# Optimization experiments

Measured on AMD Instinct MI355X. Metric: run time of the kernel, lower is better.

The kernel has to match this reference:

```python
import jax, jax.numpy as jnp
import numpy as np

N_NODES = 100000
N_EDGES = 1600000
F_IN = 256
HEADS1, DIM1 = 8, 8
N_CLASSES = 16
NEG_SLOPE = 0.2  # LeakyReLU slope used by GAT attention


def _gat_layer(x, src, dst, W, a_src, a_dst, n_nodes):
    """Graph attention layer (Velickovic et al.).
    x: [N, Fin], W: [Fin, H*D], a_src/a_dst: [H, D]. Returns [N, H, D].
    """
    H, D = a_src.shape
    h = (x @ W).reshape(-1, H, D)                      # [N, H, D]
    s = jnp.einsum('nhd,hd->nh', h, a_src)             # [N, H]
    t = jnp.einsum('nhd,hd->nh', h, a_dst)             # [N, H]
    e = jax.nn.leaky_relu(s[src] + t[dst], NEG_SLOPE)  # [E, H] per-edge logits
    # numerically stable segment softmax over incoming edges of each dst node
    m = jax.ops.segment_max(e, dst, num_segments=n_nodes)
    m = jnp.where(jnp.isfinite(m), m, 0.0)
    ex = jnp.exp(e - m[dst])                           # [E, H]
    denom = jax.ops.segment_sum(ex, dst, num_segments=n_nodes)
    alpha = ex / (denom[dst] + 1e-16)                  # [E, H]
    # gather source features, weight by attention, scatter-add to dst
    out = jax.ops.segment_sum(alpha[:, :, None] * h[src], dst,
                              num_segments=n_nodes)    # [N, H, D]
    return out


def setup_inputs() -> dict:
    key = jax.random.key(0)
    ks = jax.random.split(key, 8)
    x = jax.random.normal(ks[0], (N_NODES, F_IN), dtype=jnp.float32)
    edge_index = jax.random.randint(ks[1], (2, N_EDGES), 0, N_NODES, dtype=jnp.int64)
    W1 = jax.random.normal(ks[2], (F_IN, HEADS1 * DIM1), dtype=jnp.float32) * 0.1
    a1_src = jax.random.normal(ks[3], (HEADS1, DIM1), dtype=jnp.float32) * 0.1
    a1_dst = jax.random.normal(ks[4], (HEADS1, DIM1), dtype=jnp.float32) * 0.1
    W2 = jax.random.normal(ks[5], (HEADS1 * DIM1, N_CLASSES), dtype=jnp.float32) * 0.1
    a2_src = jax.random.normal(ks[6], (1, N_CLASSES), dtype=jnp.float32) * 0.1
    a2_dst = jax.random.normal(ks[7], (1, N_CLASSES), dtype=jnp.float32) * 0.1
    return {"x": x, "edge_index": edge_index, "W1": W1, "a1_src": a1_src,
            "a1_dst": a1_dst, "W2": W2, "a2_src": a2_src, "a2_dst": a2_dst}


def reference(x, edge_index, W1, a1_src, a1_dst, W2, a2_src, a2_dst):
    # eval mode: dropout(p=0.6) layers are identity
    src, dst = edge_index[0], edge_index[1]
    h1 = _gat_layer(x, src, dst, W1, a1_src, a1_dst, N_NODES)   # [N, 8, 8]
    h1 = jax.nn.elu(h1.reshape(N_NODES, HEADS1 * DIM1))         # concat heads
    h2 = _gat_layer(h1, src, dst, W2, a2_src, a2_dst, N_NODES)  # [N, 1, C]
    logits = h2.reshape(N_NODES, N_CLASSES)
    return jax.nn.log_softmax(logits, axis=1)
```

## Files before the change

kernel.cpp:

```cpp
#include <hip/hip_runtime.h>
#include <math.h>

#define N_NODES 100000
#define N_EDGES 1600000
#define NHEAD   8
#define NC      16
#define NEG     0.2f
#define BSH     8
#define NBUCK   391
#define CAP     5120
#define TILE2   4096
#define NBLK2   391

typedef __attribute__((ext_vector_type(4))) float f32x4;
typedef __attribute__((ext_vector_type(8))) short s16x8;

__device__ __forceinline__ float lrelu(float x) { return x > 0.f ? x : NEG * x; }
__device__ __forceinline__ short bf16rne(float f) {
    unsigned u = __float_as_uint(f);
    return (short)((u + 0x7FFFu + ((u >> 16) & 1u)) >> 16);
}
__device__ __forceinline__ float bf2f(unsigned short u) {
    return __uint_as_float(((unsigned)u) << 16);
}

__global__ __launch_bounds__(256) void wtrans_kernel(const float* __restrict__ W1,
                                                     float4* __restrict__ Wt) {
    int u = blockIdx.x * 256 + threadIdx.x;
    int j = u >> 9, ks = (u >> 6) & 7, l = u & 63;
    int colc = j * 16 + (l & 15);
    int k0 = ks * 32 + (l >> 4) * 8;
    union { s16x8 s; float4 f; } pk;
#pragma unroll
    for (int i = 0; i < 8; ++i) pk.s[i] = bf16rne(W1[(size_t)(k0 + i) * 64 + colc]);
    Wt[u] = pk.f;
}

__global__ __launch_bounds__(256) void gemm1_kernel(
    const float* __restrict__ x, const float4* __restrict__ Wt,
    const float* __restrict__ a1s, const float* __restrict__ a1d,
    unsigned short* __restrict__ hb, float* __restrict__ s, float* __restrict__ t) {
    __shared__ float4 WtL[2048];
    int tid = threadIdx.x;
#pragma unroll
    for (int i = 0; i < 8; ++i) WtL[tid + i * 256] = Wt[tid + i * 256];
    int w = tid >> 6, lane = tid & 63;
    int n0 = blockIdx.x * 128;
    int r0 = n0 + w * 32 + (lane & 15);
    int r1 = r0 + 16;
    int cr0 = r0 < N_NODES ? r0 : 0;
    int cr1 = r1 < N_NODES ? r1 : 0;
    int koff = (lane >> 4) * 8;
    f32x4 acc[2][4];
#pragma unroll
    for (int r = 0; r < 2; ++r)
#pragma unroll
        for (int j = 0; j < 4; ++j) acc[r][j] = (f32x4)0.f;
    __syncthreads();
#pragma unroll
    for (int ks = 0; ks < 8; ++ks) {
        const float* p0 = x + (size_t)cr0 * 256 + ks * 32 + koff;
        const float* p1 = x + (size_t)cr1 * 256 + ks * 32 + koff;
        float4 a0l = *(const float4*)p0, a0h = *(const float4*)(p0 + 4);
        float4 a1l = *(const float4*)p1, a1h = *(const float4*)(p1 + 4);
        s16x8 A0, A1;
        A0[0] = bf16rne(a0l.x); A0[1] = bf16rne(a0l.y); A0[2] = bf16rne(a0l.z); A0[3] = bf16rne(a0l.w);
        A0[4] = bf16rne(a0h.x); A0[5] = bf16rne(a0h.y); A0[6] = bf16rne(a0h.z); A0[7] = bf16rne(a0h.w);
        A1[0] = bf16rne(a1l.x); A1[1] = bf16rne(a1l.y); A1[2] = bf16rne(a1l.z); A1[3] = bf16rne(a1l.w);
        A1[4] = bf16rne(a1h.x); A1[5] = bf16rne(a1h.y); A1[6] = bf16rne(a1h.z); A1[7] = bf16rne(a1h.w);
#pragma unroll
        for (int j = 0; j < 4; ++j) {
            s16x8 B = *(s16x8*)&WtL[(j * 8 + ks) * 64 + lane];
            acc[0][j] = __builtin_amdgcn_mfma_f32_16x16x32_bf16(A0, B, acc[0][j], 0, 0, 0);
            acc[1][j] = __builtin_amdgcn_mfma_f32_16x16x32_bf16(A1, B, acc[1][j], 0, 0, 0);
        }
    }
    float asv[4], adv[4];
#pragma unroll
    for (int j = 0; j < 4; ++j) {
        int c = j * 16 + (lane & 15);
        asv[j] = a1s[c]; adv[j] = a1d[c];
    }
    int rbase = (lane >> 4) * 4;
#pragma unroll
    for (int r = 0; r < 2; ++r) {
#pragma unroll
        for (int reg = 0; reg < 4; ++reg) {
            int grow = n0 + w * 32 + r * 16 + rbase + reg;
            bool live = grow < N_NODES;
            unsigned short* hp = hb + (size_t)grow * 64 + (lane & 15);
#pragma unroll
            for (int j = 0; j < 4; ++j) {
                float hv = acc[r][j][reg];
                if (live) hp[j * 16] = (unsigned short)bf16rne(hv);
                float ps = hv * asv[j];
                float pt = hv * adv[j];
                ps += __shfl_xor(ps, 1, 64); ps += __shfl_xor(ps, 2, 64); ps += __shfl_xor(ps, 4, 64);
                pt += __shfl_xor(pt, 1, 64); pt += __shfl_xor(pt, 2, 64); pt += __shfl_xor(pt, 4, 64);
                if ((lane & 7) == 0 && live) {
                    int head = 2 * j + ((lane >> 3) & 1);
                    s[grow * 8 + head] = ps;
                    t[grow * 8 + head] = pt;
                }
            }
        }
    }
}

__global__ __launch_bounds__(512) void binscatter_kernel(
    const int* __restrict__ esrc, const int* __restrict__ edst,
    int* __restrict__ bcur, unsigned* __restrict__ tmp) {
    __shared__ unsigned buf[TILE2];
    __shared__ int hist[512], lbase[512], cur[512], gbase[512];
    int tid = threadIdx.x;
    hist[tid] = 0; cur[tid] = 0;
    __syncthreads();
    int e0 = blockIdx.x * TILE2;
#pragma unroll
    for (int k = 0; k < TILE2 / 512; ++k) {
        int e = e0 + k * 512 + tid;
        if (e < N_EDGES) atomicAdd(&hist[edst[e] >> BSH], 1);
    }
    __syncthreads();
    int v = hist[tid];
    lbase[tid] = v;
    __syncthreads();
    for (int off = 1; off < 512; off <<= 1) {
        int a = (tid >= off) ? lbase[tid - off] : 0;
        __syncthreads();
        lbase[tid] += a;
        __syncthreads();
    }
    lbase[tid] -= v;
    gbase[tid] = v ? atomicAdd(&bcur[tid], v) : 0;
    __syncthreads();
#pragma unroll
    for (int k = 0; k < TILE2 / 512; ++k) {
        int e = e0 + k * 512 + tid;
        if (e < N_EDGES) {
            int d = edst[e];
            int b = d >> BSH;
            int p = lbase[b] + atomicAdd(&cur[b], 1);
            buf[p] = (unsigned)esrc[e] | ((unsigned)(d & ((1 << BSH) - 1)) << 17);
        }
    }
    __syncthreads();
    int w = tid >> 6, lane = tid & 63;
    for (int b = w; b < 512; b += 8) {
        int L = hist[b];
        if (!L) continue;
        int lb = lbase[b];
        size_t base = (size_t)b * CAP + gbase[b];
        for (int i = lane; i < L; i += 64) tmp[base + i] = buf[lb + i];
    }
}

__global__ __launch_bounds__(256) void bsort_kernel(
    const int* __restrict__ bcur, const unsigned* __restrict__ tmp,
    int* __restrict__ rowbeg, int* __restrict__ rowend, int* __restrict__ colslab) {
    __shared__ unsigned sorted[CAP];
    __shared__ int cnt[256], scn[256];
    int tid = threadIdx.x, b = blockIdx.x;
    int L = bcur[b];
    const unsigned* tb = tmp + (size_t)b * CAP;
    cnt[tid] = 0;
    __syncthreads();
    for (int i = tid; i < L; i += 256) atomicAdd(&cnt[tb[i] >> 17], 1);
    __syncthreads();
    int v = cnt[tid];
    scn[tid] = v;
    __syncthreads();
    for (int off = 1; off < 256; off <<= 1) {
        int a = (tid >= off) ? scn[tid - off] : 0;
        __syncthreads();
        scn[tid] += a;
        __syncthreads();
    }
    int ex = scn[tid] - v;
    int node = (b << BSH) + tid;
    if (node < N_NODES) {
        rowbeg[node] = b * CAP + ex;
        rowend[node] = b * CAP + ex + v;
    }
    cnt[tid] = ex;
    __syncthreads();
    for (int i = tid; i < L; i += 256) {
        unsigned u = tb[i];
        int p = atomicAdd(&cnt[u >> 17], 1);
        sorted[p] = u & 0x1FFFFu;
    }
    __syncthreads();
    for (int i = tid; i < L; i += 256) colslab[(size_t)b * CAP + i] = (int)sorted[i];
}

__global__ __launch_bounds__(256) void agg1_kernel(
    const int* __restrict__ rowbeg, const int* __restrict__ rowend,
    const int* __restrict__ colslab,
    const float* __restrict__ s, const float* __restrict__ t,
    const unsigned short* __restrict__ hb, unsigned short* __restrict__ h1b) {
    int tid = threadIdx.x;
    int d = __builtin_amdgcn_readfirstlane(blockIdx.x * 4 + (tid >> 6));
    int lane = tid & 63, hh = lane >> 3;
    int beg = rowbeg[d], end = rowend[d];
    unsigned len = (unsigned)(end - beg);
    float tv = t[d * 8 + hh];
    float acc0 = 0.f, acc1 = 0.f, acc2 = 0.f, acc3 = 0.f;
    float den0 = 0.f, den1 = 0.f, den2 = 0.f, den3 = 0.f;
    for (int p = beg & ~3; p < end; p += 4) {
        int4 c4 = *(const int4*)(colslab + p);
        {
            bool ok = (unsigned)(p - beg) < len;
            int s0 = c4.x & 0x1FFFF; if (s0 >= N_NODES) s0 = 0;
            float e = __expf(lrelu(s[s0 * 8 + hh] + tv));
            e = ok ? e : 0.f;
            acc0 += e * bf2f(hb[(size_t)s0 * 64 + lane]); den0 += e;
        }
        {
            bool ok = (unsigned)(p + 1 - beg) < len;
            int s0 = c4.y & 0x1FFFF; if (s0 >= N_NODES) s0 = 0;
            float e = __expf(lrelu(s[s0 * 8 + hh] + tv));
            e = ok ? e : 0.f;
            acc1 += e * bf2f(hb[(size_t)s0 * 64 + lane]); den1 += e;
        }
        {
            bool ok = (unsigned)(p + 2 - beg) < len;
            int s0 = c4.z & 0x1FFFF; if (s0 >= N_NODES) s0 = 0;
            float e = __expf(lrelu(s[s0 * 8 + hh] + tv));
            e = ok ? e : 0.f;
            acc2 += e * bf2f(hb[(size_t)s0 * 64 + lane]); den2 += e;
        }
        {
            bool ok = (unsigned)(p + 3 - beg) < len;
            int s0 = c4.w & 0x1FFFF; if (s0 >= N_NODES) s0 = 0;
            float e = __expf(lrelu(s[s0 * 8 + hh] + tv));
            e = ok ? e : 0.f;
            acc3 += e * bf2f(hb[(size_t)s0 * 64 + lane]); den3 += e;
        }
    }
    float v = (acc0 + acc1 + acc2 + acc3) / (den0 + den1 + den2 + den3 + 1e-16f);
    float r = v > 0.f ? v : __expf(v) - 1.f;
    h1b[(size_t)d * 64 + lane] = (unsigned short)bf16rne(r);
}

__global__ __launch_bounds__(256) void gemm2_kernel(
    const unsigned short* __restrict__ h1b, const float* __restrict__ W2,
    const float* __restrict__ a2s, const float* __restrict__ a2d,
    unsigned short* __restrict__ h2b, float* __restrict__ s2, float* __restrict__ t2) {
    __shared__ float Wl[64 * NC];
    __shared__ float h1l[16 * 65];
    int tid = threadIdx.x;
    ((float4*)Wl)[tid] = ((const float4*)W2)[tid];
    {
        uint2 raw = ((const uint2*)h1b)[(size_t)blockIdx.x * 256 + tid];
        int f = tid * 4, rr = f >> 6, kk = f & 63;
        float* dp = &h1l[rr * 65 + kk];
        dp[0] = __uint_as_float(raw.x << 16);
        dp[1] = __uint_as_float(raw.x & 0xFFFF0000u);
        dp[2] = __uint_as_float(raw.y << 16);
        dp[3] = __uint_as_float(raw.y & 0xFFFF0000u);
    }
    __syncthreads();
    int c = tid & 15, r = tid >> 4;
    int n = blockIdx.x * 16 + r;
    float a = 0.f;
#pragma unroll 16
    for (int k = 0; k < 64; ++k) a += h1l[r * 65 + k] * Wl[k * NC + c];
    h2b[(size_t)n * NC + c] = (unsigned short)bf16rne(a);
    float vs = a * a2s[c];
    float vt = a * a2d[c];
#pragma unroll
    for (int o = 1; o < 16; o <<= 1) {
        vs += __shfl_xor(vs, o, 64);
        vt += __shfl_xor(vt, o, 64);
    }
    if (c == 0) { s2[n] = vs; t2[n] = vt; }
}

__global__ __launch_bounds__(256) void agg2_kernel(
    const int* __restrict__ rowbeg, const int* __restrict__ rowend,
    const int* __restrict__ colslab,
    const float* __restrict__ s2, const float* __restrict__ t2,
    const unsigned short* __restrict__ h2b, float* __restrict__ out) {
    int tid = threadIdx.x;
    int d = blockIdx.x * 16 + (tid >> 4);
    int c = tid & 15;
    int beg = rowbeg[d], end = rowend[d];
    unsigned len = (unsigned)(end - beg);
    float tv = t2[d];
    float acc0 = 0.f, acc1 = 0.f, acc2 = 0.f, acc3 = 0.f;
    float den0 = 0.f, den1 = 0.f, den2 = 0.f, den3 = 0.f;
    for (int p = beg & ~3; p < end; p += 4) {
        int4 c4 = *(const int4*)(colslab + p);
        {
            bool ok = (unsigned)(p - beg) < len;
            int s0 = c4.x & 0x1FFFF; if (s0 >= N_NODES) s0 = 0;
            float e = __expf(lrelu(s2[s0] + tv));
            e = ok ? e : 0.f;
            acc0 += e * bf2f(h2b[(size_t)s0 * 16 + c]); den0 += e;
        }
        {
            bool ok = (unsigned)(p + 1 - beg) < len;
            int s0 = c4.y & 0x1FFFF; if (s0 >= N_NODES) s0 = 0;
            float e = __expf(lrelu(s2[s0] + tv));
            e = ok ? e : 0.f;
            acc1 += e * bf2f(h2b[(size_t)s0 * 16 + c]); den1 += e;
        }
        {
            bool ok = (unsigned)(p + 2 - beg) < len;
            int s0 = c4.z & 0x1FFFF; if (s0 >= N_NODES) s0 = 0;
            float e = __expf(lrelu(s2[s0] + tv));
            e = ok ? e : 0.f;
            acc2 += e * bf2f(h2b[(size_t)s0 * 16 + c]); den2 += e;
        }
        {
            bool ok = (unsigned)(p + 3 - beg) < len;
            int s0 = c4.w & 0x1FFFF; if (s0 >= N_NODES) s0 = 0;
            float e = __expf(lrelu(s2[s0] + tv));
            e = ok ? e : 0.f;
            acc3 += e * bf2f(h2b[(size_t)s0 * 16 + c]); den3 += e;
        }
    }
    float v = (acc0 + acc1 + acc2 + acc3) / (den0 + den1 + den2 + den3 + 1e-16f);
    float mx = v;
#pragma unroll
    for (int o = 1; o < 16; o <<= 1) mx = fmaxf(mx, __shfl_xor(mx, o, 64));
    float e = __expf(v - mx), sum = e;
#pragma unroll
    for (int o = 1; o < 16; o <<= 1) sum += __shfl_xor(sum, o, 64);
    out[(size_t)d * NC + c] = v - mx - __logf(sum);
}

extern "C" void kernel_launch(void* const* d_in, const int* in_sizes, int n_in,
                              void* d_out, int out_size, void* d_ws, size_t ws_size,
                              hipStream_t stream) {
    const float* x   = (const float*)d_in[0];
    const int*  eidx = (const int*)d_in[1];
    const float* W1  = (const float*)d_in[2];
    const float* a1s = (const float*)d_in[3];
    const float* a1d = (const float*)d_in[4];
    const float* W2  = (const float*)d_in[5];
    const float* a2s = (const float*)d_in[6];
    const float* a2d = (const float*)d_in[7];
    float* out = (float*)d_out;
    const int* esrc = eidx;
    const int* edst = eidx + N_EDGES;

    char* p = (char*)d_ws;
    int*      bcur    = (int*)p;      p += 512 * 4;
    unsigned* tmp     = (unsigned*)p; p += (size_t)NBUCK * CAP * 4;
    int*      colslab = (int*)p;      p += (size_t)NBUCK * CAP * 4 + 64;
    int*      rowbeg  = (int*)p;      p += (size_t)N_NODES * 4;
    int*      rowend  = (int*)p;      p += (size_t)N_NODES * 4;
    float4*   Wt      = (float4*)p;   p += (size_t)2048 * 16;
    unsigned short* hb  = (unsigned short*)p; p += (size_t)N_NODES * 64 * 2;
    float*    s       = (float*)p;    p += (size_t)N_NODES * 8 * 4;
    float*    t       = (float*)p;    p += (size_t)N_NODES * 8 * 4;
    unsigned short* h1b = (unsigned short*)p; p += (size_t)N_NODES * 64 * 2;
    unsigned short* h2b = (unsigned short*)p; p += (size_t)N_NODES * NC * 2;
    float*    s2      = (float*)p;    p += (size_t)N_NODES * 4;
    float*    t2      = (float*)p;    p += (size_t)N_NODES * 4;

    hipMemsetAsync(bcur, 0, 512 * 4, stream);

    wtrans_kernel<<<8, 256, 0, stream>>>(W1, Wt);
    gemm1_kernel<<<(N_NODES + 127) / 128, 256, 0, stream>>>(x, Wt, a1s, a1d, hb, s, t);
    binscatter_kernel<<<NBLK2, 512, 0, stream>>>(esrc, edst, bcur, tmp);
    bsort_kernel<<<NBUCK, 256, 0, stream>>>(bcur, tmp, rowbeg, rowend, colslab);
    agg1_kernel<<<N_NODES / 4, 256, 0, stream>>>(rowbeg, rowend, colslab, s, t, hb, h1b);
    gemm2_kernel<<<N_NODES / 16, 256, 0, stream>>>(h1b, W2, a2s, a2d, h2b, s2, t2);
    agg2_kernel<<<N_NODES / 16, 256, 0, stream>>>(rowbeg, rowend, colslab, s2, t2, h2b, out);
}
```

Measured before the change: 347.3 us.

## Compute edge softmax weights once per lane and broadcast via shuffles; use wave-shuffle scans

In both aggregation kernels, each lane now loads one edge's source index and computes that edge's attention exponent once. The values are then broadcast across the group with shuffles, where before every feature lane recomputed the exp and reloaded the score for every edge. This removes roughly 8x (layer 1) and 16x (layer 2) redundant exp and score gathers, at the cost of extra shuffle instructions and possible reads of colslab past the row end. Separately, the LDS Hillis-Steele prefix scans in the binning and bucket-sort kernels are replaced by in-wave shuffle scans plus a small per-wave sum, which cuts many block barriers.

After: 342.9 us. About the same (-1.3%).

```diff
diff --git a/kernel.cpp b/kernel.cpp
--- a/kernel.cpp
+++ b/kernel.cpp
@@ -111,7 +111,7 @@
     const int* __restrict__ esrc, const int* __restrict__ edst,
     int* __restrict__ bcur, unsigned* __restrict__ tmp) {
     __shared__ unsigned buf[TILE2];
-    __shared__ int hist[512], lbase[512], cur[512], gbase[512];
+    __shared__ int hist[512], lbase[512], cur[512], gbase[512], wsum[8];
     int tid = threadIdx.x;
     hist[tid] = 0; cur[tid] = 0;
     __syncthreads();
@@ -123,15 +123,18 @@
     }
     __syncthreads();
     int v = hist[tid];
-    lbase[tid] = v;
-    __syncthreads();
-    for (int off = 1; off < 512; off <<= 1) {
-        int a = (tid >= off) ? lbase[tid - off] : 0;
-        __syncthreads();
-        lbase[tid] += a;
-        __syncthreads();
-    }
-    lbase[tid] -= v;
+    int w = tid >> 6, lane = tid & 63;
+    int inc = v;
+#pragma unroll
+    for (int off = 1; off < 64; off <<= 1) {
+        int nb = __shfl_up(inc, off, 64);
+        if (lane >= off) inc += nb;
+    }
+    if (lane == 63) wsum[w] = inc;
+    __syncthreads();
+    int woff = 0;
+    for (int k = 0; k < w; ++k) woff += wsum[k];
+    lbase[tid] = inc - v + woff;
     gbase[tid] = v ? atomicAdd(&bcur[tid], v) : 0;
     __syncthreads();
 #pragma unroll
@@ -145,7 +148,6 @@
         }
     }
     __syncthreads();
-    int w = tid >> 6, lane = tid & 63;
     for (int b = w; b < 512; b += 8) {
         int L = hist[b];
         if (!L) continue;
@@ -159,7 +161,8 @@
     const int* __restrict__ bcur, const unsigned* __restrict__ tmp,
     int* __restrict__ rowbeg, int* __restrict__ rowend, int* __restrict__ colslab) {
     __shared__ unsigned sorted[CAP];
-    __shared__ int cnt[256], scn[256];
+    __shared__ int cnt[256];
+    __shared__ int wsum[4];
     int tid = threadIdx.x, b = blockIdx.x;
     int L = bcur[b];
     const unsigned* tb = tmp + (size_t)b * CAP;
@@ -168,15 +171,18 @@
     for (int i = tid; i < L; i += 256) atomicAdd(&cnt[tb[i] >> 17], 1);
     __syncthreads();
     int v = cnt[tid];
-    scn[tid] = v;
-    __syncthreads();
-    for (int off = 1; off < 256; off <<= 1) {
-        int a = (tid >= off) ? scn[tid - off] : 0;
-        __syncthreads();
-        scn[tid] += a;
-        __syncthreads();
-    }
-    int ex = scn[tid] - v;
+    int w = tid >> 6, lane = tid & 63;
+    int inc = v;
+#pragma unroll
+    for (int off = 1; off < 64; off <<= 1) {
+        int nb = __shfl_up(inc, off, 64);
+        if (lane >= off) inc += nb;
+    }
+    if (lane == 63) wsum[w] = inc;
+    __syncthreads();
+    int woff = 0;
+    for (int k = 0; k < w; ++k) woff += wsum[k];
+    int ex = inc - v + woff;
     int node = (b << BSH) + tid;
     if (node < N_NODES) {
         rowbeg[node] = b * CAP + ex;
@@ -200,44 +206,30 @@
     const unsigned short* __restrict__ hb, unsigned short* __restrict__ h1b) {
     int tid = threadIdx.x;
     int d = __builtin_amdgcn_readfirstlane(blockIdx.x * 4 + (tid >> 6));
-    int lane = tid & 63, hh = lane >> 3;
+    int lane = tid & 63;
+    int hh = lane >> 3;
+    int hA = lane & 7;
+    int sub = lane >> 3;
     int beg = rowbeg[d], end = rowend[d];
-    unsigned len = (unsigned)(end - beg);
-    float tv = t[d * 8 + hh];
-    float acc0 = 0.f, acc1 = 0.f, acc2 = 0.f, acc3 = 0.f;
-    float den0 = 0.f, den1 = 0.f, den2 = 0.f, den3 = 0.f;
-    for (int p = beg & ~3; p < end; p += 4) {
-        int4 c4 = *(const int4*)(colslab + p);
-        {
-            bool ok = (unsigned)(p - beg) < len;
-            int s0 = c4.x & 0x1FFFF; if (s0 >= N_NODES) s0 = 0;
-            float e = __expf(lrelu(s[s0 * 8 + hh] + tv));
-            e = ok ? e : 0.f;
-            acc0 += e * bf2f(hb[(size_t)s0 * 64 + lane]); den0 += e;
-        }
-        {
-            bool ok = (unsigned)(p + 1 - beg) < len;
-            int s0 = c4.y & 0x1FFFF; if (s0 >= N_NODES) s0 = 0;
-            float e = __expf(lrelu(s[s0 * 8 + hh] + tv));
-            e = ok ? e : 0.f;
-            acc1 += e * bf2f(hb[(size_t)s0 * 64 + lane]); den1 += e;
-        }
-        {
-            bool ok = (unsigned)(p + 2 - beg) < len;
-            int s0 = c4.z & 0x1FFFF; if (s0 >= N_NODES) s0 = 0;
-            float e = __expf(lrelu(s[s0 * 8 + hh] + tv));
-            e = ok ? e : 0.f;
-            acc2 += e * bf2f(hb[(size_t)s0 * 64 + lane]); den2 += e;
-        }
-        {
-            bool ok = (unsigned)(p + 3 - beg) < len;
-            int s0 = c4.w & 0x1FFFF; if (s0 >= N_NODES) s0 = 0;
-            float e = __expf(lrelu(s[s0 * 8 + hh] + tv));
-            e = ok ? e : 0.f;
-            acc3 += e * bf2f(hb[(size_t)s0 * 64 + lane]); den3 += e;
-        }
-    }
-    float v = (acc0 + acc1 + acc2 + acc3) / (den0 + den1 + den2 + den3 + 1e-16f);
+    float tvA = t[d * 8 + hA];
+    float acc[4] = {0.f, 0.f, 0.f, 0.f};
+    float den[4] = {0.f, 0.f, 0.f, 0.f};
+    for (int p = beg; p < end; p += 8) {
+        int pe = p + sub;
+        int s0 = colslab[pe];
+        if ((unsigned)s0 >= N_NODES) s0 = 0;
+        float ev = __expf(lrelu(s[s0 * 8 + hA] + tvA));
+        ev = (pe < end) ? ev : 0.f;
+#pragma unroll
+        for (int j = 0; j < 8; ++j) {
+            float e = __shfl(ev, j * 8 + hh, 64);
+            int sj  = __shfl(s0, j * 8, 64);
+            acc[j & 3] += e * bf2f(hb[(size_t)sj * 64 + lane]);
+            den[j & 3] += e;
+        }
+    }
+    float v = (acc[0] + acc[1] + acc[2] + acc[3])
+            / (den[0] + den[1] + den[2] + den[3] + 1e-16f);
     float r = v > 0.f ? v : __expf(v) - 1.f;
     h1b[(size_t)d * 64 + lane] = (unsigned short)bf16rne(r);
 }
@@ -283,44 +275,29 @@
     const unsigned short* __restrict__ h2b, float* __restrict__ out) {
     int tid = threadIdx.x;
     int d = blockIdx.x * 16 + (tid >> 4);
-    int c = tid & 15;
+    int lane = tid & 63;
+    int c = lane & 15;
+    int gb = lane & 48;
     int beg = rowbeg[d], end = rowend[d];
-    unsigned len = (unsigned)(end - beg);
     float tv = t2[d];
-    float acc0 = 0.f, acc1 = 0.f, acc2 = 0.f, acc3 = 0.f;
-    float den0 = 0.f, den1 = 0.f, den2 = 0.f, den3 = 0.f;
-    for (int p = beg & ~3; p < end; p += 4) {
-        int4 c4 = *(const int4*)(colslab + p);
-        {
-            bool ok = (unsigned)(p - beg) < len;
-            int s0 = c4.x & 0x1FFFF; if (s0 >= N_NODES) s0 = 0;
-            float e = __expf(lrelu(s2[s0] + tv));
-            e = ok ? e : 0.f;
-            acc0 += e * bf2f(h2b[(size_t)s0 * 16 + c]); den0 += e;
-        }
-        {
-            bool ok = (unsigned)(p + 1 - beg) < len;
-            int s0 = c4.y & 0x1FFFF; if (s0 >= N_NODES) s0 = 0;
-            float e = __expf(lrelu(s2[s0] + tv));
-            e = ok ? e : 0.f;
-            acc1 += e * bf2f(h2b[(size_t)s0 * 16 + c]); den1 += e;
-        }
-        {
-            bool ok = (unsigned)(p + 2 - beg) < len;
-            int s0 = c4.z & 0x1FFFF; if (s0 >= N_NODES) s0 = 0;
-            float e = __expf(lrelu(s2[s0] + tv));
-            e = ok ? e : 0.f;
-            acc2 += e * bf2f(h2b[(size_t)s0 * 16 + c]); den2 += e;
-        }
-        {
-            bool ok = (unsigned)(p + 3 - beg) < len;
-            int s0 = c4.w & 0x1FFFF; if (s0 >= N_NODES) s0 = 0;
-            float e = __expf(lrelu(s2[s0] + tv));
-            e = ok ? e : 0.f;
-            acc3 += e * bf2f(h2b[(size_t)s0 * 16 + c]); den3 += e;
-        }
-    }
-    float v = (acc0 + acc1 + acc2 + acc3) / (den0 + den1 + den2 + den3 + 1e-16f);
+    float acc[4] = {0.f, 0.f, 0.f, 0.f};
+    float den[4] = {0.f, 0.f, 0.f, 0.f};
+    for (int p = beg; p < end; p += 16) {
+        int pe = p + c;
+        int s0 = colslab[pe];
+        if ((unsigned)s0 >= N_NODES) s0 = 0;
+        float ev = __expf(lrelu(s2[s0] + tv));
+        ev = (pe < end) ? ev : 0.f;
+#pragma unroll
+        for (int j = 0; j < 16; ++j) {
+            float e = __shfl(ev, gb + j, 64);
+            int sj  = __shfl(s0, gb + j, 64);
+            acc[j & 3] += e * bf2f(h2b[(size_t)sj * 16 + c]);
+            den[j & 3] += e;
+        }
+    }
+    float v = (acc[0] + acc[1] + acc[2] + acc[3])
+            / (den[0] + den[1] + den[2] + den[3] + 1e-16f);
     float mx = v;
 #pragma unroll
     for (int o = 1; o < 16; o <<= 1) mx = fmaxf(mx, __shfl_xor(mx, o, 64));
```
